# Kernel tuning notes

Hardware: AMD Instinct MI355X
Metric: run time of the kernel (lower is better)

The kernel has to match this reference:

```python
import jax, jax.numpy as jnp
import numpy as np

N_EDGES = 4096
HIDDEN = 256
EDGE_DIM = 128
NUM_HEADS = 4
NUM_GRAPHS = 64


def setup_inputs() -> dict:
    key0 = jax.random.key(0)
    ks = jax.random.split(key0, 10)
    s = 0.02
    inp = {
        "query": jax.random.normal(ks[0], (N_EDGES, HIDDEN), jnp.float32),
        "key": jax.random.normal(ks[1], (N_EDGES, EDGE_DIM), jnp.float32),
        "value": jax.random.normal(ks[2], (N_EDGES, EDGE_DIM), jnp.float32),
        "edge_graph_index": jnp.sort(
            jax.random.randint(ks[3], (N_EDGES,), 0, NUM_GRAPHS)
        ),
        # edge_proj: Linear(edge_context_dim -> hidden_dim)
        "w_edge": jax.random.normal(ks[4], (HIDDEN, EDGE_DIM), jnp.float32) * s,
        "b_edge": jnp.zeros((HIDDEN,), jnp.float32),
        # nn.MultiheadAttention packed in-projection [3H, H] and bias [3H]
        "w_in": jax.random.normal(ks[5], (3 * HIDDEN, HIDDEN), jnp.float32) * s,
        "b_in": jnp.zeros((3 * HIDDEN,), jnp.float32),
        # out_proj: Linear(hidden -> hidden)
        "w_out": jax.random.normal(ks[6], (HIDDEN, HIDDEN), jnp.float32) * s,
        "b_out": jnp.zeros((HIDDEN,), jnp.float32),
    }
    return inp


def reference(query, key, value, edge_graph_index,
              w_edge, b_edge, w_in, b_in, w_out, b_out):
    # Segment-wise cross attention == block-diagonal masked attention over all edges.
    N, H = query.shape
    nh = NUM_HEADS
    dh = H // nh

    # edge feature projection (applied to both key and value, as in the module)
    K = key @ w_edge.T + b_edge      # [N, H]
    V = value @ w_edge.T + b_edge    # [N, H]

    wq, wk, wv = jnp.split(w_in, 3, axis=0)
    bq, bk, bv = jnp.split(b_in, 3)
    Qh = (query @ wq.T + bq).reshape(N, nh, dh)
    Kh = (K @ wk.T + bk).reshape(N, nh, dh)
    Vh = (V @ wv.T + bv).reshape(N, nh, dh)

    scale = 1.0 / jnp.sqrt(jnp.asarray(dh, query.dtype))
    scores = jnp.einsum("nhd,mhd->hnm", Qh, Kh) * scale  # [nh, N, N]

    # attention only within the same graph segment
    same_graph = edge_graph_index[:, None] == edge_graph_index[None, :]  # [N, N]
    neg = jnp.finfo(scores.dtype).min
    scores = jnp.where(same_graph[None, :, :], scores, neg)

    attn = jax.nn.softmax(scores, axis=-1)                 # [nh, N, N]
    out = jnp.einsum("hnm,mhd->nhd", attn, Vh).reshape(N, H)
    out = out @ w_out.T + b_out
    return query + out
```

## Files before the change

### kernel.cpp

```cpp
#include <hip/hip_runtime.h>

#define N_EDGES 4096
#define HIDDEN  256
#define EDGE_DIM 128
#define NUM_HEADS 4
#define NUM_GRAPHS 64
#define DH 64

typedef __attribute__((ext_vector_type(8))) short short8;
typedef __attribute__((ext_vector_type(4))) float f32x4;

__device__ __forceinline__ unsigned short f2bf(float f) {
  unsigned u = __builtin_bit_cast(unsigned, f);
  u += 0x7FFF + ((u >> 16) & 1);
  return (unsigned short)(u >> 16);
}
__device__ __forceinline__ float bf2f(unsigned short u) {
  return __builtin_bit_cast(float, (unsigned)u << 16);
}
__device__ __forceinline__ short8 cvt8(float4 x, float4 y) {
  short8 v;
  v[0] = (short)f2bf(x.x); v[1] = (short)f2bf(x.y);
  v[2] = (short)f2bf(x.z); v[3] = (short)f2bf(x.w);
  v[4] = (short)f2bf(y.x); v[5] = (short)f2bf(y.y);
  v[6] = (short)f2bf(y.z); v[7] = (short)f2bf(y.w);
  return v;
}
__device__ __forceinline__ float4 us4f(ushort4 v) {
  float4 f;
  f.x = bf2f(v.x); f.y = bf2f(v.y); f.z = bf2f(v.z); f.w = bf2f(v.w);
  return f;
}

__device__ __forceinline__ int lbound(const int* __restrict__ a, int n, int v) {
  int lo = 0, hi = n;
  while (lo < hi) { int mid = (lo + hi) >> 1; if (a[mid] < v) lo = mid + 1; else hi = mid; }
  return lo;
}

template<bool ABF, bool OUTF32>
__device__ __forceinline__ void gemm_core(const void* Ap, const float* W,
                                          const float* bias, const float* res,
                                          void* Cp, const int K) {
  const int t = threadIdx.x;
  const int m0 = blockIdx.x * 64, n0 = blockIdx.y * 64;
  __shared__ unsigned short As[64 * 40];
  __shared__ unsigned short Ws[64 * 40];
  const int r = t >> 2, kg = t & 3;
  const int lane = t & 63, w = t >> 6;
  const int quad = lane >> 4, l16 = lane & 15;
  const int wm = (w >> 1) * 32, wn = (w & 1) * 32;
  f32x4 acc[2][2] = {};
  const float* pw = W + (size_t)(n0 + r) * K + kg * 8;
  float4 w0 = *(const float4*)(pw), w1 = *(const float4*)(pw + 4);
  const unsigned short* pa16 = (const unsigned short*)Ap + (size_t)(m0 + r) * K + kg * 8;
  const float* pa32 = (const float*)Ap + (size_t)(m0 + r) * K + kg * 8;
  short8 a16; float4 a0, a1;
  if (ABF) a16 = *(const short8*)pa16;
  else { a0 = *(const float4*)pa32; a1 = *(const float4*)(pa32 + 4); }
  for (int kc = 0; kc < K; kc += 32) {
    short8 na16; float4 na0, na1, nw0, nw1;
    if (kc + 32 < K) {
      if (ABF) na16 = *(const short8*)(pa16 + kc + 32);
      else { na0 = *(const float4*)(pa32 + kc + 32); na1 = *(const float4*)(pa32 + kc + 36); }
      nw0 = *(const float4*)(pw + kc + 32); nw1 = *(const float4*)(pw + kc + 36);
    }
    __syncthreads();
    short8 av = ABF ? a16 : cvt8(a0, a1);
    *(short8*)&As[r * 40 + kg * 8] = av;
    *(short8*)&Ws[r * 40 + kg * 8] = cvt8(w0, w1);
    __syncthreads();
    short8 af0 = *(const short8*)&As[(wm + l16) * 40 + quad * 8];
    short8 af1 = *(const short8*)&As[(wm + 16 + l16) * 40 + quad * 8];
    short8 bf0 = *(const short8*)&Ws[(wn + l16) * 40 + quad * 8];
    short8 bf1 = *(const short8*)&Ws[(wn + 16 + l16) * 40 + quad * 8];
    acc[0][0] = __builtin_amdgcn_mfma_f32_16x16x32_bf16(af0, bf0, acc[0][0], 0, 0, 0);
    acc[0][1] = __builtin_amdgcn_mfma_f32_16x16x32_bf16(af0, bf1, acc[0][1], 0, 0, 0);
    acc[1][0] = __builtin_amdgcn_mfma_f32_16x16x32_bf16(af1, bf0, acc[1][0], 0, 0, 0);
    acc[1][1] = __builtin_amdgcn_mfma_f32_16x16x32_bf16(af1, bf1, acc[1][1], 0, 0, 0);
    a16 = na16; a0 = na0; a1 = na1; w0 = nw0; w1 = nw1;
  }
#pragma unroll
  for (int j = 0; j < 2; ++j) {
    const int col = n0 + wn + j * 16 + l16;
    const float bj = bias[col];
#pragma unroll
    for (int i = 0; i < 2; ++i) {
#pragma unroll
      for (int reg = 0; reg < 4; ++reg) {
        const int row = m0 + wm + i * 16 + quad * 4 + reg;
        const size_t idx = (size_t)row * HIDDEN + col;
        float v = acc[i][j][reg] + bj;
        if (OUTF32) ((float*)Cp)[idx] = v + res[idx];
        else        ((unsigned short*)Cp)[idx] = f2bf(v);
      }
    }
  }
}

__global__ __launch_bounds__(256) void proj1(const float* __restrict__ query,
                                             const float* __restrict__ key,
                                             const float* __restrict__ value,
                                             const float* __restrict__ w_in,
                                             const float* __restrict__ b_in,
                                             const float* __restrict__ w_edge,
                                             const float* __restrict__ b_edge,
                                             const int* __restrict__ gidx,
                                             unsigned short* Qh, unsigned short* Ek,
                                             unsigned short* Ev, int* segStart) {
  if (blockIdx.z == 0 && blockIdx.x == 0 && blockIdx.y == 0 && threadIdx.x <= NUM_GRAPHS)
    segStart[threadIdx.x] = lbound(gidx, N_EDGES, threadIdx.x);
  if (blockIdx.z == 0)      gemm_core<false, false>(query, w_in,   b_in,   nullptr, Qh, 256);
  else if (blockIdx.z == 1) gemm_core<false, false>(key,   w_edge, b_edge, nullptr, Ek, 128);
  else                      gemm_core<false, false>(value, w_edge, b_edge, nullptr, Ev, 128);
}

__global__ __launch_bounds__(256) void proj2(const unsigned short* __restrict__ Ek,
                                             const unsigned short* __restrict__ Ev,
                                             const float* __restrict__ w_in,
                                             const float* __restrict__ b_in,
                                             unsigned short* Kh, unsigned short* Vh) {
  if (blockIdx.z == 0) gemm_core<true, false>(Ek, w_in + 256 * HIDDEN, b_in + 256, nullptr, Kh, 256);
  else                 gemm_core<true, false>(Ev, w_in + 512 * HIDDEN, b_in + 512, nullptr, Vh, 256);
}

__global__ __launch_bounds__(256) void attn_segment(const unsigned short* __restrict__ Qh,
                                                    const unsigned short* __restrict__ Kh,
                                                    const unsigned short* __restrict__ Vh,
                                                    const int* __restrict__ segStart,
                                                    unsigned short* __restrict__ ao) {
  const int graph = blockIdx.x, h = blockIdx.y, zg = blockIdx.z;
  const int segLo = segStart[graph];
  const int segHi = segStart[graph + 1];
  const int segLen = segHi - segLo;
  const int t = threadIdx.x, lane = t & 63, w = t >> 6;
  __shared__ float Qs[16][68], Ks[64][68], Vs[64][68];
  __shared__ float Ps[4][64][4];
  const float scale = 0.125f;
  const int r0 = w * 4;

  for (int chunk = zg; chunk * 16 < segLen; chunk += 8) {
    const int row0 = segLo + chunk * 16;
    const int rows = min(16, segHi - row0);
    __syncthreads();
    { int r = t >> 4, d4 = (t & 15) * 4;
      if (r < rows)
        *(float4*)&Qs[r][d4] =
            us4f(*(const ushort4*)(Qh + (size_t)(row0 + r) * HIDDEN + h * DH + d4)); }

    float accv[4] = {0.f, 0.f, 0.f, 0.f}, lsum[4] = {0.f, 0.f, 0.f, 0.f};

    for (int c0 = segLo; c0 < segHi; c0 += 64) {
      const int tc = min(64, segHi - c0);
      __syncthreads();
#pragma unroll
      for (int it = 0; it < 4; ++it) {
        int s = t + it * 256; int j = s >> 4; int d4 = (s & 15) * 4;
        if (j < tc) {
          *(float4*)&Ks[j][d4] =
              us4f(*(const ushort4*)(Kh + (size_t)(c0 + j) * HIDDEN + h * DH + d4));
          *(float4*)&Vs[j][d4] =
              us4f(*(const ushort4*)(Vh + (size_t)(c0 + j) * HIDDEN + h * DH + d4));
        }
      }
      __syncthreads();
      float4 kreg[16];
#pragma unroll
      for (int d4 = 0; d4 < 16; ++d4) kreg[d4] = *(const float4*)&Ks[lane][d4 * 4];
      float p[4];
#pragma unroll
      for (int r = 0; r < 4; ++r) {
        float s = 0.f;
#pragma unroll
        for (int d4 = 0; d4 < 16; ++d4) {
          float4 q = *(const float4*)&Qs[r0 + r][d4 * 4];
          s += q.x * kreg[d4].x + q.y * kreg[d4].y + q.z * kreg[d4].z + q.w * kreg[d4].w;
        }
        p[r] = (lane < tc && r0 + r < rows) ? __expf(s * scale) : 0.f;
        lsum[r] += p[r];
      }
      float4 p4; p4.x = p[0]; p4.y = p[1]; p4.z = p[2]; p4.w = p[3];
      *(float4*)&Ps[w][lane][0] = p4;
      __asm__ volatile("s_waitcnt lgkmcnt(0)" ::: "memory");
      for (int j = 0; j < tc; ++j) {
        const float v = Vs[j][lane];
        float4 pj = *(const float4*)&Ps[w][j][0];
        accv[0] += pj.x * v; accv[1] += pj.y * v;
        accv[2] += pj.z * v; accv[3] += pj.w * v;
      }
    }
#pragma unroll
    for (int off = 32; off; off >>= 1)
#pragma unroll
      for (int r = 0; r < 4; ++r) lsum[r] += __shfl_xor(lsum[r], off);
#pragma unroll
    for (int r = 0; r < 4; ++r)
      if (r0 + r < rows)
        ao[(size_t)(row0 + r0 + r) * HIDDEN + h * DH + lane] = f2bf(accv[r] / lsum[r]);
  }
}

__global__ __launch_bounds__(256) void outproj(const unsigned short* __restrict__ ao,
                                               const float* __restrict__ w_out,
                                               const float* __restrict__ b_out,
                                               const float* __restrict__ query,
                                               float* __restrict__ out) {
  gemm_core<true, true>(ao, w_out, b_out, query, out, 256);
}

extern "C" void kernel_launch(void* const* d_in, const int* in_sizes, int n_in,
                              void* d_out, int out_size, void* d_ws, size_t ws_size,
                              hipStream_t stream) {
  const float* query  = (const float*)d_in[0];
  const float* key    = (const float*)d_in[1];
  const float* value  = (const float*)d_in[2];
  const int*   gidx   = (const int*)d_in[3];
  const float* w_edge = (const float*)d_in[4];
  const float* b_edge = (const float*)d_in[5];
  const float* w_in   = (const float*)d_in[6];
  const float* b_in   = (const float*)d_in[7];
  const float* w_out  = (const float*)d_in[8];
  const float* b_out  = (const float*)d_in[9];
  float* out = (float*)d_out;

  int* segStart = (int*)d_ws;
  unsigned short* Qh = (unsigned short*)((char*)d_ws + 512);
  unsigned short* Ek = Qh + (size_t)N_EDGES * HIDDEN;
  unsigned short* Ev = Ek + (size_t)N_EDGES * HIDDEN;
  unsigned short* Kh = Ev + (size_t)N_EDGES * HIDDEN;
  unsigned short* Vh = Kh + (size_t)N_EDGES * HIDDEN;
  unsigned short* ao = Vh + (size_t)N_EDGES * HIDDEN;

  proj1<<<dim3(64, 4, 3), 256, 0, stream>>>(query, key, value, w_in, b_in,
                                            w_edge, b_edge, gidx, Qh, Ek, Ev, segStart);
  proj2<<<dim3(64, 4, 2), 256, 0, stream>>>(Ek, Ev, w_in, b_in, Kh, Vh);
  attn_segment<<<dim3(NUM_GRAPHS, NUM_HEADS, 8), 256, 0, stream>>>(Qh, Kh, Vh, segStart, ao);
  outproj<<<dim3(64, 4), 256, 0, stream>>>(ao, w_out, b_out, query, out);
}
```

Measured before the change: 117.7 us.

## Fold edge and in-projections per block, fuse out-projection into attention via atomics

The K/V path now multiplies the two weight matrices inside each block (W_in_k @ W_edge, with a folded bias) and applies the product directly to key/value. This removes the separate proj2 launch and the intermediate Ek/Ev buffers. The output projection is fused into the attention kernel: each head chunk multiplies its bf16 output by the matching slice of w_out and atomically adds into out, which proj pre-initialises with query plus b_out. The change drops two launches and two round trips through global memory, but every block recomputes the weight product, fp32 atomics add contention, and accumulation order becomes nondeterministic.

```diff
diff --git a/kernel.cpp b/kernel.cpp
--- a/kernel.cpp
+++ b/kernel.cpp
@@ -38,10 +38,9 @@
   return lo;
 }
 
-template<bool ABF, bool OUTF32>
-__device__ __forceinline__ void gemm_core(const void* Ap, const float* W,
-                                          const float* bias, const float* res,
-                                          void* Cp, const int K) {
+__device__ __forceinline__ void gemm_core(const float* Ap, const float* W,
+                                          const float* bias, unsigned short* Cp,
+                                          const int K) {
   const int t = threadIdx.x;
   const int m0 = blockIdx.x * 64, n0 = blockIdx.y * 64;
   __shared__ unsigned short As[64 * 40];
@@ -53,21 +52,16 @@
   f32x4 acc[2][2] = {};
   const float* pw = W + (size_t)(n0 + r) * K + kg * 8;
   float4 w0 = *(const float4*)(pw), w1 = *(const float4*)(pw + 4);
-  const unsigned short* pa16 = (const unsigned short*)Ap + (size_t)(m0 + r) * K + kg * 8;
-  const float* pa32 = (const float*)Ap + (size_t)(m0 + r) * K + kg * 8;
-  short8 a16; float4 a0, a1;
-  if (ABF) a16 = *(const short8*)pa16;
-  else { a0 = *(const float4*)pa32; a1 = *(const float4*)(pa32 + 4); }
+  const float* pa32 = Ap + (size_t)(m0 + r) * K + kg * 8;
+  float4 a0 = *(const float4*)pa32, a1 = *(const float4*)(pa32 + 4);
   for (int kc = 0; kc < K; kc += 32) {
-    short8 na16; float4 na0, na1, nw0, nw1;
+    float4 na0, na1, nw0, nw1;
     if (kc + 32 < K) {
-      if (ABF) na16 = *(const short8*)(pa16 + kc + 32);
-      else { na0 = *(const float4*)(pa32 + kc + 32); na1 = *(const float4*)(pa32 + kc + 36); }
-      nw0 = *(const float4*)(pw + kc + 32); nw1 = *(const float4*)(pw + kc + 36);
-    }
-    __syncthreads();
-    short8 av = ABF ? a16 : cvt8(a0, a1);
-    *(short8*)&As[r * 40 + kg * 8] = av;
+      na0 = *(const float4*)(pa32 + kc + 32); na1 = *(const float4*)(pa32 + kc + 36);
+      nw0 = *(const float4*)(pw + kc + 32);   nw1 = *(const float4*)(pw + kc + 36);
+    }
+    __syncthreads();
+    *(short8*)&As[r * 40 + kg * 8] = cvt8(a0, a1);
     *(short8*)&Ws[r * 40 + kg * 8] = cvt8(w0, w1);
     __syncthreads();
     short8 af0 = *(const short8*)&As[(wm + l16) * 40 + quad * 8];
@@ -78,7 +72,7 @@
     acc[0][1] = __builtin_amdgcn_mfma_f32_16x16x32_bf16(af0, bf1, acc[0][1], 0, 0, 0);
     acc[1][0] = __builtin_amdgcn_mfma_f32_16x16x32_bf16(af1, bf0, acc[1][0], 0, 0, 0);
     acc[1][1] = __builtin_amdgcn_mfma_f32_16x16x32_bf16(af1, bf1, acc[1][1], 0, 0, 0);
-    a16 = na16; a0 = na0; a1 = na1; w0 = nw0; w1 = nw1;
+    a0 = na0; a1 = na1; w0 = nw0; w1 = nw1;
   }
 #pragma unroll
   for (int j = 0; j < 2; ++j) {
@@ -89,53 +83,164 @@
 #pragma unroll
       for (int reg = 0; reg < 4; ++reg) {
         const int row = m0 + wm + i * 16 + quad * 4 + reg;
-        const size_t idx = (size_t)row * HIDDEN + col;
-        float v = acc[i][j][reg] + bj;
-        if (OUTF32) ((float*)Cp)[idx] = v + res[idx];
-        else        ((unsigned short*)Cp)[idx] = f2bf(v);
-      }
-    }
-  }
-}
-
-__global__ __launch_bounds__(256) void proj1(const float* __restrict__ query,
-                                             const float* __restrict__ key,
-                                             const float* __restrict__ value,
-                                             const float* __restrict__ w_in,
-                                             const float* __restrict__ b_in,
-                                             const float* __restrict__ w_edge,
-                                             const float* __restrict__ b_edge,
-                                             const int* __restrict__ gidx,
-                                             unsigned short* Qh, unsigned short* Ek,
-                                             unsigned short* Ev, int* segStart) {
-  if (blockIdx.z == 0 && blockIdx.x == 0 && blockIdx.y == 0 && threadIdx.x <= NUM_GRAPHS)
-    segStart[threadIdx.x] = lbound(gidx, N_EDGES, threadIdx.x);
-  if (blockIdx.z == 0)      gemm_core<false, false>(query, w_in,   b_in,   nullptr, Qh, 256);
-  else if (blockIdx.z == 1) gemm_core<false, false>(key,   w_edge, b_edge, nullptr, Ek, 128);
-  else                      gemm_core<false, false>(value, w_edge, b_edge, nullptr, Ev, 128);
-}
-
-__global__ __launch_bounds__(256) void proj2(const unsigned short* __restrict__ Ek,
-                                             const unsigned short* __restrict__ Ev,
-                                             const float* __restrict__ w_in,
-                                             const float* __restrict__ b_in,
-                                             unsigned short* Kh, unsigned short* Vh) {
-  if (blockIdx.z == 0) gemm_core<true, false>(Ek, w_in + 256 * HIDDEN, b_in + 256, nullptr, Kh, 256);
-  else                 gemm_core<true, false>(Ev, w_in + 512 * HIDDEN, b_in + 512, nullptr, Vh, 256);
+        Cp[(size_t)row * HIDDEN + col] = f2bf(acc[i][j][reg] + bj);
+      }
+    }
+  }
+}
+
+__device__ __forceinline__ void fused_kv_core(const float* __restrict__ A,
+                                              const float* __restrict__ Wp,
+                                              const float* __restrict__ bp,
+                                              const float* __restrict__ w_edge,
+                                              const float* __restrict__ b_edge,
+                                              unsigned short* __restrict__ C) {
+  const int t = threadIdx.x;
+  const int m0 = blockIdx.x * 64, n0 = blockIdx.y * 64;
+  __shared__ unsigned short As2[64 * 40];
+  __shared__ unsigned short Bs2[64 * 40];
+  __shared__ unsigned short WfS[64][136];
+  __shared__ float bfS[64];
+  const int r = t >> 2, kg = t & 3;
+  const int lane = t & 63, w = t >> 6;
+  const int quad = lane >> 4, l16 = lane & 15;
+  const int wm = (w >> 1) * 32, wn = (w & 1) * 32;
+
+  {
+    float s = 0.f;
+    const float* wrow = Wp + (size_t)(n0 + r) * HIDDEN + kg * 64;
+    const float* be = b_edge + kg * 64;
+#pragma unroll
+    for (int j = 0; j < 64; j += 4) {
+      float4 a = *(const float4*)(wrow + j);
+      float4 b = *(const float4*)(be + j);
+      s += a.x * b.x + a.y * b.y + a.z * b.z + a.w * b.w;
+    }
+    s += __shfl_xor(s, 1); s += __shfl_xor(s, 2);
+    if (kg == 0) bfS[r] = s + bp[n0 + r];
+  }
+
+#pragma unroll
+  for (int kt = 0; kt < 2; ++kt) {
+    f32x4 facc[2][2] = {};
+    for (int j0 = 0; j0 < HIDDEN; j0 += 32) {
+      __syncthreads();
+      {
+        const float* p = Wp + (size_t)(n0 + r) * HIDDEN + j0 + kg * 8;
+        float4 a0 = *(const float4*)p, a1 = *(const float4*)(p + 4);
+        *(short8*)&As2[r * 40 + kg * 8] = cvt8(a0, a1);
+      }
+      {
+        const int j = t >> 3, k8 = (t & 7) * 8;
+        const float* p = w_edge + (size_t)(j0 + j) * EDGE_DIM + kt * 64 + k8;
+        float4 b0 = *(const float4*)p, b1 = *(const float4*)(p + 4);
+        float bb[8] = {b0.x, b0.y, b0.z, b0.w, b1.x, b1.y, b1.z, b1.w};
+#pragma unroll
+        for (int i = 0; i < 8; ++i) Bs2[(k8 + i) * 40 + j] = f2bf(bb[i]);
+      }
+      __syncthreads();
+      short8 af0 = *(const short8*)&As2[(wm + l16) * 40 + quad * 8];
+      short8 af1 = *(const short8*)&As2[(wm + 16 + l16) * 40 + quad * 8];
+      short8 bf0 = *(const short8*)&Bs2[(wn + l16) * 40 + quad * 8];
+      short8 bf1 = *(const short8*)&Bs2[(wn + 16 + l16) * 40 + quad * 8];
+      facc[0][0] = __builtin_amdgcn_mfma_f32_16x16x32_bf16(af0, bf0, facc[0][0], 0, 0, 0);
+      facc[0][1] = __builtin_amdgcn_mfma_f32_16x16x32_bf16(af0, bf1, facc[0][1], 0, 0, 0);
+      facc[1][0] = __builtin_amdgcn_mfma_f32_16x16x32_bf16(af1, bf0, facc[1][0], 0, 0, 0);
+      facc[1][1] = __builtin_amdgcn_mfma_f32_16x16x32_bf16(af1, bf1, facc[1][1], 0, 0, 0);
+    }
+#pragma unroll
+    for (int jj = 0; jj < 2; ++jj)
+#pragma unroll
+      for (int ii = 0; ii < 2; ++ii)
+#pragma unroll
+        for (int reg = 0; reg < 4; ++reg) {
+          const int n = wm + ii * 16 + quad * 4 + reg;
+          const int k = kt * 64 + wn + jj * 16 + l16;
+          WfS[n][k] = f2bf(facc[ii][jj][reg]);
+        }
+  }
+  __syncthreads();
+
+  f32x4 acc[2][2] = {};
+  for (int kc = 0; kc < EDGE_DIM; kc += 32) {
+    __syncthreads();
+    {
+      const float* p = A + (size_t)(m0 + r) * EDGE_DIM + kc + kg * 8;
+      float4 a0 = *(const float4*)p, a1 = *(const float4*)(p + 4);
+      *(short8*)&As2[r * 40 + kg * 8] = cvt8(a0, a1);
+    }
+    __syncthreads();
+    short8 af0 = *(const short8*)&As2[(wm + l16) * 40 + quad * 8];
+    short8 af1 = *(const short8*)&As2[(wm + 16 + l16) * 40 + quad * 8];
+    short8 bf0 = *(const short8*)&WfS[wn + l16][kc + quad * 8];
+    short8 bf1 = *(const short8*)&WfS[wn + 16 + l16][kc + quad * 8];
+    acc[0][0] = __builtin_amdgcn_mfma_f32_16x16x32_bf16(af0, bf0, acc[0][0], 0, 0, 0);
+    acc[0][1] = __builtin_amdgcn_mfma_f32_16x16x32_bf16(af0, bf1, acc[0][1], 0, 0, 0);
+    acc[1][0] = __builtin_amdgcn_mfma_f32_16x16x32_bf16(af1, bf0, acc[1][0], 0, 0, 0);
+    acc[1][1] = __builtin_amdgcn_mfma_f32_16x16x32_bf16(af1, bf1, acc[1][1], 0, 0, 0);
+  }
+#pragma unroll
+  for (int j = 0; j < 2; ++j) {
+    const int coln = wn + j * 16 + l16;
+    const float bj = bfS[coln];
+#pragma unroll
+    for (int i = 0; i < 2; ++i)
+#pragma unroll
+      for (int reg = 0; reg < 4; ++reg) {
+        const int row = m0 + wm + i * 16 + quad * 4 + reg;
+        C[(size_t)row * HIDDEN + n0 + coln] = f2bf(acc[i][j][reg] + bj);
+      }
+  }
+}
+
+__global__ __launch_bounds__(256) void proj(const float* __restrict__ query,
+                                            const float* __restrict__ key,
+                                            const float* __restrict__ value,
+                                            const float* __restrict__ w_in,
+                                            const float* __restrict__ b_in,
+                                            const float* __restrict__ w_edge,
+                                            const float* __restrict__ b_edge,
+                                            const float* __restrict__ b_out,
+                                            const int* __restrict__ gidx,
+                                            unsigned short* Qh, unsigned short* Kh,
+                                            unsigned short* Vh, int* segStart,
+                                            float* __restrict__ out) {
+  if (blockIdx.z == 0) {
+    if (blockIdx.x == 0 && blockIdx.y == 0 && threadIdx.x <= NUM_GRAPHS)
+      segStart[threadIdx.x] = lbound(gidx, N_EDGES, threadIdx.x);
+    gemm_core(query, w_in, b_in, Qh, 256);
+    const int t = threadIdx.x, m0 = blockIdx.x * 64, n0 = blockIdx.y * 64;
+#pragma unroll
+    for (int i = 0; i < 4; ++i) {
+      const int idx = t + i * 256;
+      const int rr = idx >> 4, cc = (idx & 15) * 4;
+      float4 q = *(const float4*)&query[(size_t)(m0 + rr) * HIDDEN + n0 + cc];
+      float4 b = *(const float4*)&b_out[n0 + cc];
+      q.x += b.x; q.y += b.y; q.z += b.z; q.w += b.w;
+      *(float4*)&out[(size_t)(m0 + rr) * HIDDEN + n0 + cc] = q;
+    }
+  } else if (blockIdx.z == 1) {
+    fused_kv_core(key, w_in + 256 * HIDDEN, b_in + 256, w_edge, b_edge, Kh);
+  } else {
+    fused_kv_core(value, w_in + 512 * HIDDEN, b_in + 512, w_edge, b_edge, Vh);
+  }
 }
 
 __global__ __launch_bounds__(256) void attn_segment(const unsigned short* __restrict__ Qh,
                                                     const unsigned short* __restrict__ Kh,
                                                     const unsigned short* __restrict__ Vh,
                                                     const int* __restrict__ segStart,
-                                                    unsigned short* __restrict__ ao) {
+                                                    const float* __restrict__ w_out,
+                                                    float* __restrict__ out) {
   const int graph = blockIdx.x, h = blockIdx.y, zg = blockIdx.z;
   const int segLo = segStart[graph];
   const int segHi = segStart[graph + 1];
   const int segLen = segHi - segLo;
   const int t = threadIdx.x, lane = t & 63, w = t >> 6;
+  const int quad = lane >> 4, l16 = lane & 15;
   __shared__ float Qs[16][68], Ks[64][68], Vs[64][68];
   __shared__ float Ps[4][64][4];
+  __shared__ unsigned short aohS[16][72];
   const float scale = 0.125f;
   const int r0 = w * 4;
 
@@ -193,19 +298,34 @@
     for (int off = 32; off; off >>= 1)
 #pragma unroll
       for (int r = 0; r < 4; ++r) lsum[r] += __shfl_xor(lsum[r], off);
+
 #pragma unroll
     for (int r = 0; r < 4; ++r)
-      if (r0 + r < rows)
-        ao[(size_t)(row0 + r0 + r) * HIDDEN + h * DH + lane] = f2bf(accv[r] / lsum[r]);
-  }
-}
-
-__global__ __launch_bounds__(256) void outproj(const unsigned short* __restrict__ ao,
-                                               const float* __restrict__ w_out,
-                                               const float* __restrict__ b_out,
-                                               const float* __restrict__ query,
-                                               float* __restrict__ out) {
-  gemm_core<true, true>(ao, w_out, b_out, query, out, 256);
+      aohS[r0 + r][lane] = (r0 + r < rows) ? f2bf(accv[r] / lsum[r]) : (unsigned short)0;
+    __syncthreads();
+
+    f32x4 po[4] = {};
+#pragma unroll
+    for (int kc = 0; kc < DH; kc += 32) {
+      short8 af = *(const short8*)&aohS[l16][kc + quad * 8];
+#pragma unroll
+      for (int nt = 0; nt < 4; ++nt) {
+        const int n = w * 64 + nt * 16 + l16;
+        const float* p = w_out + (size_t)n * HIDDEN + h * DH + kc + quad * 8;
+        float4 b0 = *(const float4*)p, b1 = *(const float4*)(p + 4);
+        po[nt] = __builtin_amdgcn_mfma_f32_16x16x32_bf16(af, cvt8(b0, b1), po[nt], 0, 0, 0);
+      }
+    }
+#pragma unroll
+    for (int nt = 0; nt < 4; ++nt)
+#pragma unroll
+      for (int reg = 0; reg < 4; ++reg) {
+        const int rr = quad * 4 + reg;
+        if (rr < rows)
+          atomicAdd(&out[(size_t)(row0 + rr) * HIDDEN + w * 64 + nt * 16 + l16],
+                    po[nt][reg]);
+      }
+  }
 }
 
 extern "C" void kernel_launch(void* const* d_in, const int* in_sizes, int n_in,
@@ -225,15 +345,12 @@
 
   int* segStart = (int*)d_ws;
   unsigned short* Qh = (unsigned short*)((char*)d_ws + 512);
-  unsigned short* Ek = Qh + (size_t)N_EDGES * HIDDEN;
-  unsigned short* Ev = Ek + (size_t)N_EDGES * HIDDEN;
-  unsigned short* Kh = Ev + (size_t)N_EDGES * HIDDEN;
+  unsigned short* Kh = Qh + (size_t)N_EDGES * HIDDEN;
   unsigned short* Vh = Kh + (size_t)N_EDGES * HIDDEN;
-  unsigned short* ao = Vh + (size_t)N_EDGES * HIDDEN;
-
-  proj1<<<dim3(64, 4, 3), 256, 0, stream>>>(query, key, value, w_in, b_in,
-                                            w_edge, b_edge, gidx, Qh, Ek, Ev, segStart);
-  proj2<<<dim3(64, 4, 2), 256, 0, stream>>>(Ek, Ev, w_in, b_in, Kh, Vh);
-  attn_segment<<<dim3(NUM_GRAPHS, NUM_HEADS, 8), 256, 0, stream>>>(Qh, Kh, Vh, segStart, ao);
-  outproj<<<dim3(64, 4), 256, 0, stream>>>(ao, w_out, b_out, query, out);
-}
+
+  proj<<<dim3(64, 4, 3), 256, 0, stream>>>(query, key, value, w_in, b_in,
+                                           w_edge, b_edge, b_out, gidx,
+                                           Qh, Kh, Vh, segStart, out);
+  attn_segment<<<dim3(NUM_GRAPHS, NUM_HEADS, 8), 256, 0, stream>>>(Qh, Kh, Vh, segStart,
+                                                                   w_out, out);
+}
```

Measured after the change: 135.2 us. +14.9%, slower.

## Fold edge projection into K/V in-projection weights and fuse stages into cooperative kernel

Applied to the files above, without the earlier changes.

Precomputes the fused weights Wk·W_edge and Wv·W_edge (plus fused biases) on device, so K and V are produced by a single K=128 GEMM from the raw key/value instead of two chained GEMMs. All stages run inside one persistent cooperative kernel of 512 blocks separated by grid syncs, removing three kernel launch boundaries. The attention work is spread over the persistent blocks in a strided loop. A multi-kernel fallback runs if the cooperative launch fails. It adds the risk of extra bf16 rounding in the fused weights and a dependence on 512 blocks being co-resident.

```diff
diff --git a/kernel.cpp b/kernel.cpp
--- a/kernel.cpp
+++ b/kernel.cpp
@@ -1,4 +1,7 @@
 #include <hip/hip_runtime.h>
+#include <hip/hip_cooperative_groups.h>
+
+namespace cg = cooperative_groups;
 
 #define N_EDGES 4096
 #define HIDDEN  256
@@ -6,6 +9,8 @@
 #define NUM_HEADS 4
 #define NUM_GRAPHS 64
 #define DH 64
+#define NBLK 512
+#define ATTN_UNITS 2048
 
 typedef __attribute__((ext_vector_type(8))) short short8;
 typedef __attribute__((ext_vector_type(4))) float f32x4;
@@ -38,47 +43,54 @@
   return lo;
 }
 
-template<bool ABF, bool OUTF32>
-__device__ __forceinline__ void gemm_core(const void* Ap, const float* W,
-                                          const float* bias, const float* res,
-                                          void* Cp, const int K) {
+union SharedU {
+  struct { unsigned short As[64 * 40]; unsigned short Ws[64 * 40]; } g;
+  struct { float Qs[16][68]; float Ks[64][68]; float Vs[64][68]; float Ps[4][64][4]; } a;
+};
+
+template<bool ABF, bool WBF, bool OUTF32>
+__device__ __forceinline__ void gemm_tile(const void* Ap, const void* Wp,
+                                          const float* __restrict__ bias,
+                                          const float* __restrict__ res,
+                                          void* Cp, const int K,
+                                          const int m0, const int n0,
+                                          unsigned short* As, unsigned short* Ws) {
   const int t = threadIdx.x;
-  const int m0 = blockIdx.x * 64, n0 = blockIdx.y * 64;
-  __shared__ unsigned short As[64 * 40];
-  __shared__ unsigned short Ws[64 * 40];
   const int r = t >> 2, kg = t & 3;
   const int lane = t & 63, w = t >> 6;
   const int quad = lane >> 4, l16 = lane & 15;
   const int wm = (w >> 1) * 32, wn = (w & 1) * 32;
   f32x4 acc[2][2] = {};
-  const float* pw = W + (size_t)(n0 + r) * K + kg * 8;
-  float4 w0 = *(const float4*)(pw), w1 = *(const float4*)(pw + 4);
+  const float*          pa32 = (const float*)Ap          + (size_t)(m0 + r) * K + kg * 8;
   const unsigned short* pa16 = (const unsigned short*)Ap + (size_t)(m0 + r) * K + kg * 8;
-  const float* pa32 = (const float*)Ap + (size_t)(m0 + r) * K + kg * 8;
-  short8 a16; float4 a0, a1;
+  const float*          pw32 = (const float*)Wp          + (size_t)(n0 + r) * K + kg * 8;
+  const unsigned short* pw16 = (const unsigned short*)Wp + (size_t)(n0 + r) * K + kg * 8;
+  short8 a16, w16; float4 a0, a1, w0, w1;
   if (ABF) a16 = *(const short8*)pa16;
   else { a0 = *(const float4*)pa32; a1 = *(const float4*)(pa32 + 4); }
+  if (WBF) w16 = *(const short8*)pw16;
+  else { w0 = *(const float4*)pw32; w1 = *(const float4*)(pw32 + 4); }
   for (int kc = 0; kc < K; kc += 32) {
-    short8 na16; float4 na0, na1, nw0, nw1;
+    short8 na16, nw16; float4 na0, na1, nw0, nw1;
     if (kc + 32 < K) {
       if (ABF) na16 = *(const short8*)(pa16 + kc + 32);
       else { na0 = *(const float4*)(pa32 + kc + 32); na1 = *(const float4*)(pa32 + kc + 36); }
-      nw0 = *(const float4*)(pw + kc + 32); nw1 = *(const float4*)(pw + kc + 36);
+      if (WBF) nw16 = *(const short8*)(pw16 + kc + 32);
+      else { nw0 = *(const float4*)(pw32 + kc + 32); nw1 = *(const float4*)(pw32 + kc + 36); }
     }
     __syncthreads();
-    short8 av = ABF ? a16 : cvt8(a0, a1);
-    *(short8*)&As[r * 40 + kg * 8] = av;
-    *(short8*)&Ws[r * 40 + kg * 8] = cvt8(w0, w1);
+    *(short8*)&As[r * 40 + kg * 8] = ABF ? a16 : cvt8(a0, a1);
+    *(short8*)&Ws[r * 40 + kg * 8] = WBF ? w16 : cvt8(w0, w1);
     __syncthreads();
     short8 af0 = *(const short8*)&As[(wm + l16) * 40 + quad * 8];
     short8 af1 = *(const short8*)&As[(wm + 16 + l16) * 40 + quad * 8];
-    short8 bf0 = *(const short8*)&Ws[(wn + l16) * 40 + quad * 8];
-    short8 bf1 = *(const short8*)&Ws[(wn + 16 + l16) * 40 + quad * 8];
-    acc[0][0] = __builtin_amdgcn_mfma_f32_16x16x32_bf16(af0, bf0, acc[0][0], 0, 0, 0);
-    acc[0][1] = __builtin_amdgcn_mfma_f32_16x16x32_bf16(af0, bf1, acc[0][1], 0, 0, 0);
-    acc[1][0] = __builtin_amdgcn_mfma_f32_16x16x32_bf16(af1, bf0, acc[1][0], 0, 0, 0);
-    acc[1][1] = __builtin_amdgcn_mfma_f32_16x16x32_bf16(af1, bf1, acc[1][1], 0, 0, 0);
-    a16 = na16; a0 = na0; a1 = na1; w0 = nw0; w1 = nw1;
+    short8 bq0 = *(const short8*)&Ws[(wn + l16) * 40 + quad * 8];
+    short8 bq1 = *(const short8*)&Ws[(wn + 16 + l16) * 40 + quad * 8];
+    acc[0][0] = __builtin_amdgcn_mfma_f32_16x16x32_bf16(af0, bq0, acc[0][0], 0, 0, 0);
+    acc[0][1] = __builtin_amdgcn_mfma_f32_16x16x32_bf16(af0, bq1, acc[0][1], 0, 0, 0);
+    acc[1][0] = __builtin_amdgcn_mfma_f32_16x16x32_bf16(af1, bq0, acc[1][0], 0, 0, 0);
+    acc[1][1] = __builtin_amdgcn_mfma_f32_16x16x32_bf16(af1, bq1, acc[1][1], 0, 0, 0);
+    a16 = na16; a0 = na0; a1 = na1; w16 = nw16; w0 = nw0; w1 = nw1;
   }
 #pragma unroll
   for (int j = 0; j < 2; ++j) {
@@ -98,44 +110,85 @@
   }
 }
 
-__global__ __launch_bounds__(256) void proj1(const float* __restrict__ query,
-                                             const float* __restrict__ key,
-                                             const float* __restrict__ value,
-                                             const float* __restrict__ w_in,
-                                             const float* __restrict__ b_in,
-                                             const float* __restrict__ w_edge,
-                                             const float* __restrict__ b_edge,
-                                             const int* __restrict__ gidx,
-                                             unsigned short* Qh, unsigned short* Ek,
-                                             unsigned short* Ev, int* segStart) {
-  if (blockIdx.z == 0 && blockIdx.x == 0 && blockIdx.y == 0 && threadIdx.x <= NUM_GRAPHS)
-    segStart[threadIdx.x] = lbound(gidx, N_EDGES, threadIdx.x);
-  if (blockIdx.z == 0)      gemm_core<false, false>(query, w_in,   b_in,   nullptr, Qh, 256);
-  else if (blockIdx.z == 1) gemm_core<false, false>(key,   w_edge, b_edge, nullptr, Ek, 128);
-  else                      gemm_core<false, false>(value, w_edge, b_edge, nullptr, Ev, 128);
-}
-
-__global__ __launch_bounds__(256) void proj2(const unsigned short* __restrict__ Ek,
-                                             const unsigned short* __restrict__ Ev,
-                                             const float* __restrict__ w_in,
-                                             const float* __restrict__ b_in,
-                                             unsigned short* Kh, unsigned short* Vh) {
-  if (blockIdx.z == 0) gemm_core<true, false>(Ek, w_in + 256 * HIDDEN, b_in + 256, nullptr, Kh, 256);
-  else                 gemm_core<true, false>(Ev, w_in + 512 * HIDDEN, b_in + 512, nullptr, Vh, 256);
-}
-
-__global__ __launch_bounds__(256) void attn_segment(const unsigned short* __restrict__ Qh,
-                                                    const unsigned short* __restrict__ Kh,
-                                                    const unsigned short* __restrict__ Vh,
-                                                    const int* __restrict__ segStart,
-                                                    unsigned short* __restrict__ ao) {
-  const int graph = blockIdx.x, h = blockIdx.y, zg = blockIdx.z;
+__device__ __forceinline__ void wf_part(int bb, const float* __restrict__ w_in,
+                                        const float* __restrict__ b_in,
+                                        const float* __restrict__ w_edge,
+                                        const float* __restrict__ b_edge,
+                                        unsigned short* __restrict__ Wfk,
+                                        unsigned short* __restrict__ Wfv,
+                                        float* __restrict__ bfk, float* __restrict__ bfv,
+                                        unsigned short* As, unsigned short* Bs) {
+  const int sel = bb >> 3;
+  const int tt  = bb & 7;
+  const int n0  = (tt >> 1) * 64;
+  const int k0  = (tt & 1) * 64;
+  const float* Wp = w_in + (size_t)(256 + 256 * sel) * HIDDEN;
+  const float* bp = b_in + 256 + 256 * sel;
+  unsigned short* Wf = sel ? Wfv : Wfk;
+  float* bf = sel ? bfv : bfk;
+  const int t = threadIdx.x;
+  const int r = t >> 2, kg = t & 3;
+  const int lane = t & 63, w = t >> 6;
+  const int quad = lane >> 4, l16 = lane & 15;
+  const int wm = (w >> 1) * 32, wn = (w & 1) * 32;
+  if (k0 == 0) {
+    float s = 0.f;
+    const float* wrow = Wp + (size_t)(n0 + r) * HIDDEN + kg * 64;
+    const float* be = b_edge + kg * 64;
+#pragma unroll
+    for (int j = 0; j < 64; j += 4) {
+      float4 a = *(const float4*)(wrow + j);
+      float4 b = *(const float4*)(be + j);
+      s += a.x * b.x + a.y * b.y + a.z * b.z + a.w * b.w;
+    }
+    s += __shfl_xor(s, 1); s += __shfl_xor(s, 2);
+    if (kg == 0) bf[n0 + r] = s + bp[n0 + r];
+  }
+  f32x4 facc[2][2] = {};
+  for (int j0 = 0; j0 < HIDDEN; j0 += 32) {
+    __syncthreads();
+    { const float* p = Wp + (size_t)(n0 + r) * HIDDEN + j0 + kg * 8;
+      float4 x0 = *(const float4*)p, x1 = *(const float4*)(p + 4);
+      *(short8*)&As[r * 40 + kg * 8] = cvt8(x0, x1); }
+    { const int j = t >> 3, k8 = (t & 7) * 8;
+      const float* p = w_edge + (size_t)(j0 + j) * EDGE_DIM + k0 + k8;
+      float4 b0 = *(const float4*)p, b1 = *(const float4*)(p + 4);
+      float bv[8] = {b0.x, b0.y, b0.z, b0.w, b1.x, b1.y, b1.z, b1.w};
+#pragma unroll
+      for (int i = 0; i < 8; ++i) Bs[(k8 + i) * 40 + j] = f2bf(bv[i]); }
+    __syncthreads();
+    short8 af0 = *(const short8*)&As[(wm + l16) * 40 + quad * 8];
+    short8 af1 = *(const short8*)&As[(wm + 16 + l16) * 40 + quad * 8];
+    short8 bq0 = *(const short8*)&Bs[(wn + l16) * 40 + quad * 8];
+    short8 bq1 = *(const short8*)&Bs[(wn + 16 + l16) * 40 + quad * 8];
+    facc[0][0] = __builtin_amdgcn_mfma_f32_16x16x32_bf16(af0, bq0, facc[0][0], 0, 0, 0);
+    facc[0][1] = __builtin_amdgcn_mfma_f32_16x16x32_bf16(af0, bq1, facc[0][1], 0, 0, 0);
+    facc[1][0] = __builtin_amdgcn_mfma_f32_16x16x32_bf16(af1, bq0, facc[1][0], 0, 0, 0);
+    facc[1][1] = __builtin_amdgcn_mfma_f32_16x16x32_bf16(af1, bq1, facc[1][1], 0, 0, 0);
+  }
+#pragma unroll
+  for (int jj = 0; jj < 2; ++jj)
+#pragma unroll
+    for (int ii = 0; ii < 2; ++ii)
+#pragma unroll
+      for (int reg = 0; reg < 4; ++reg) {
+        const int n = wm + ii * 16 + quad * 4 + reg;
+        const int k = wn + jj * 16 + l16;
+        Wf[(size_t)(n0 + n) * EDGE_DIM + k0 + k] = f2bf(facc[ii][jj][reg]);
+      }
+}
+
+__device__ __forceinline__ void attn_unit(int graph, int h, int zg,
+                                          const unsigned short* __restrict__ Qh,
+                                          const unsigned short* __restrict__ Kh,
+                                          const unsigned short* __restrict__ Vh,
+                                          const int* __restrict__ segStart,
+                                          unsigned short* __restrict__ ao,
+                                          SharedU& sh) {
   const int segLo = segStart[graph];
   const int segHi = segStart[graph + 1];
   const int segLen = segHi - segLo;
   const int t = threadIdx.x, lane = t & 63, w = t >> 6;
-  __shared__ float Qs[16][68], Ks[64][68], Vs[64][68];
-  __shared__ float Ps[4][64][4];
   const float scale = 0.125f;
   const int r0 = w * 4;
 
@@ -145,7 +198,7 @@
     __syncthreads();
     { int r = t >> 4, d4 = (t & 15) * 4;
       if (r < rows)
-        *(float4*)&Qs[r][d4] =
+        *(float4*)&sh.a.Qs[r][d4] =
             us4f(*(const ushort4*)(Qh + (size_t)(row0 + r) * HIDDEN + h * DH + d4)); }
 
     float accv[4] = {0.f, 0.f, 0.f, 0.f}, lsum[4] = {0.f, 0.f, 0.f, 0.f};
@@ -157,34 +210,34 @@
       for (int it = 0; it < 4; ++it) {
         int s = t + it * 256; int j = s >> 4; int d4 = (s & 15) * 4;
         if (j < tc) {
-          *(float4*)&Ks[j][d4] =
+          *(float4*)&sh.a.Ks[j][d4] =
               us4f(*(const ushort4*)(Kh + (size_t)(c0 + j) * HIDDEN + h * DH + d4));
-          *(float4*)&Vs[j][d4] =
+          *(float4*)&sh.a.Vs[j][d4] =
               us4f(*(const ushort4*)(Vh + (size_t)(c0 + j) * HIDDEN + h * DH + d4));
         }
       }
       __syncthreads();
       float4 kreg[16];
 #pragma unroll
-      for (int d4 = 0; d4 < 16; ++d4) kreg[d4] = *(const float4*)&Ks[lane][d4 * 4];
+      for (int d4 = 0; d4 < 16; ++d4) kreg[d4] = *(const float4*)&sh.a.Ks[lane][d4 * 4];
       float p[4];
 #pragma unroll
       for (int r = 0; r < 4; ++r) {
         float s = 0.f;
 #pragma unroll
         for (int d4 = 0; d4 < 16; ++d4) {
-          float4 q = *(const float4*)&Qs[r0 + r][d4 * 4];
+          float4 q = *(const float4*)&sh.a.Qs[r0 + r][d4 * 4];
           s += q.x * kreg[d4].x + q.y * kreg[d4].y + q.z * kreg[d4].z + q.w * kreg[d4].w;
         }
         p[r] = (lane < tc && r0 + r < rows) ? __expf(s * scale) : 0.f;
         lsum[r] += p[r];
       }
       float4 p4; p4.x = p[0]; p4.y = p[1]; p4.z = p[2]; p4.w = p[3];
-      *(float4*)&Ps[w][lane][0] = p4;
+      *(float4*)&sh.a.Ps[w][lane][0] = p4;
       __asm__ volatile("s_waitcnt lgkmcnt(0)" ::: "memory");
       for (int j = 0; j < tc; ++j) {
-        const float v = Vs[j][lane];
-        float4 pj = *(const float4*)&Ps[w][j][0];
+        const float v = sh.a.Vs[j][lane];
+        float4 pj = *(const float4*)&sh.a.Ps[w][j][0];
         accv[0] += pj.x * v; accv[1] += pj.y * v;
         accv[2] += pj.z * v; accv[3] += pj.w * v;
       }
@@ -200,12 +253,97 @@
   }
 }
 
-__global__ __launch_bounds__(256) void outproj(const unsigned short* __restrict__ ao,
-                                               const float* __restrict__ w_out,
-                                               const float* __restrict__ b_out,
-                                               const float* __restrict__ query,
-                                               float* __restrict__ out) {
-  gemm_core<true, true>(ao, w_out, b_out, query, out, 256);
+__global__ __launch_bounds__(256, 2) void k_all(
+    const float* __restrict__ query, const float* __restrict__ key,
+    const float* __restrict__ value, const float* __restrict__ w_in,
+    const float* __restrict__ b_in, const float* __restrict__ w_edge,
+    const float* __restrict__ b_edge, const float* __restrict__ w_out,
+    const float* __restrict__ b_out, const int* __restrict__ gidx,
+    int* segStart, unsigned short* Qh, unsigned short* Kh, unsigned short* Vh,
+    unsigned short* ao, unsigned short* Wfk, unsigned short* Wfv,
+    float* bfk, float* bfv, float* out) {
+  __shared__ SharedU sh;
+  const int b = blockIdx.x;
+  cg::grid_group grid = cg::this_grid();
+
+  if (b < 256) {
+    gemm_tile<false, false, false>(query, w_in, b_in, nullptr, Qh, 256,
+                                   (b & 63) * 64, (b >> 6) * 64, sh.g.As, sh.g.Ws);
+  } else if (b < 272) {
+    wf_part(b - 256, w_in, b_in, w_edge, b_edge, Wfk, Wfv, bfk, bfv, sh.g.As, sh.g.Ws);
+  } else if (b == 272) {
+    if (threadIdx.x <= NUM_GRAPHS)
+      segStart[threadIdx.x] = lbound(gidx, N_EDGES, threadIdx.x);
+  }
+  __threadfence();
+  grid.sync();
+
+  {
+    const int sel = b >> 8, rem = b & 255;
+    gemm_tile<false, true, false>(sel ? value : key, sel ? Wfv : Wfk,
+                                  sel ? bfv : bfk, nullptr, sel ? Vh : Kh, 128,
+                                  (rem & 63) * 64, (rem >> 6) * 64, sh.g.As, sh.g.Ws);
+  }
+  __threadfence();
+  grid.sync();
+
+  for (int u = b; u < ATTN_UNITS; u += NBLK)
+    attn_unit(u >> 5, (u >> 3) & 3, u & 7, Qh, Kh, Vh, segStart, ao, sh);
+  __threadfence();
+  grid.sync();
+
+  if (b < 256)
+    gemm_tile<true, false, true>(ao, w_out, b_out, query, out, 256,
+                                 (b & 63) * 64, (b >> 6) * 64, sh.g.As, sh.g.Ws);
+}
+
+__global__ __launch_bounds__(256) void k_p1(
+    const float* __restrict__ query, const float* __restrict__ w_in,
+    const float* __restrict__ b_in, const float* __restrict__ w_edge,
+    const float* __restrict__ b_edge, const int* __restrict__ gidx,
+    int* segStart, unsigned short* Qh, unsigned short* Wfk, unsigned short* Wfv,
+    float* bfk, float* bfv) {
+  __shared__ SharedU sh;
+  const int b = blockIdx.x;
+  if (b < 256)
+    gemm_tile<false, false, false>(query, w_in, b_in, nullptr, Qh, 256,
+                                   (b & 63) * 64, (b >> 6) * 64, sh.g.As, sh.g.Ws);
+  else if (b < 272)
+    wf_part(b - 256, w_in, b_in, w_edge, b_edge, Wfk, Wfv, bfk, bfv, sh.g.As, sh.g.Ws);
+  else if (threadIdx.x <= NUM_GRAPHS)
+    segStart[threadIdx.x] = lbound(gidx, N_EDGES, threadIdx.x);
+}
+
+__global__ __launch_bounds__(256) void k_p2(
+    const float* __restrict__ key, const float* __restrict__ value,
+    const unsigned short* __restrict__ Wfk, const unsigned short* __restrict__ Wfv,
+    const float* __restrict__ bfk, const float* __restrict__ bfv,
+    unsigned short* Kh, unsigned short* Vh) {
+  __shared__ SharedU sh;
+  const int b = blockIdx.x;
+  const int sel = b >> 8, rem = b & 255;
+  gemm_tile<false, true, false>(sel ? value : key, sel ? Wfv : Wfk,
+                                sel ? bfv : bfk, nullptr, sel ? Vh : Kh, 128,
+                                (rem & 63) * 64, (rem >> 6) * 64, sh.g.As, sh.g.Ws);
+}
+
+__global__ __launch_bounds__(256) void k_p3(
+    const unsigned short* __restrict__ Qh, const unsigned short* __restrict__ Kh,
+    const unsigned short* __restrict__ Vh, const int* __restrict__ segStart,
+    unsigned short* __restrict__ ao) {
+  __shared__ SharedU sh;
+  for (int u = blockIdx.x; u < ATTN_UNITS; u += gridDim.x)
+    attn_unit(u >> 5, (u >> 3) & 3, u & 7, Qh, Kh, Vh, segStart, ao, sh);
+}
+
+__global__ __launch_bounds__(256) void k_p4(
+    const unsigned short* __restrict__ ao, const float* __restrict__ w_out,
+    const float* __restrict__ b_out, const float* __restrict__ query,
+    float* __restrict__ out) {
+  __shared__ SharedU sh;
+  const int b = blockIdx.x;
+  gemm_tile<true, false, true>(ao, w_out, b_out, query, out, 256,
+                               (b & 63) * 64, (b >> 6) * 64, sh.g.As, sh.g.Ws);
 }
 
 extern "C" void kernel_launch(void* const* d_in, const int* in_sizes, int n_in,
@@ -224,16 +362,28 @@
   float* out = (float*)d_out;
 
   int* segStart = (int*)d_ws;
-  unsigned short* Qh = (unsigned short*)((char*)d_ws + 512);
-  unsigned short* Ek = Qh + (size_t)N_EDGES * HIDDEN;
-  unsigned short* Ev = Ek + (size_t)N_EDGES * HIDDEN;
-  unsigned short* Kh = Ev + (size_t)N_EDGES * HIDDEN;
-  unsigned short* Vh = Kh + (size_t)N_EDGES * HIDDEN;
-  unsigned short* ao = Vh + (size_t)N_EDGES * HIDDEN;
-
-  proj1<<<dim3(64, 4, 3), 256, 0, stream>>>(query, key, value, w_in, b_in,
-                                            w_edge, b_edge, gidx, Qh, Ek, Ev, segStart);
-  proj2<<<dim3(64, 4, 2), 256, 0, stream>>>(Ek, Ev, w_in, b_in, Kh, Vh);
-  attn_segment<<<dim3(NUM_GRAPHS, NUM_HEADS, 8), 256, 0, stream>>>(Qh, Kh, Vh, segStart, ao);
-  outproj<<<dim3(64, 4), 256, 0, stream>>>(ao, w_out, b_out, query, out);
-}
+  unsigned short* Qh  = (unsigned short*)((char*)d_ws + 512);
+  unsigned short* Kh  = Qh + (size_t)N_EDGES * HIDDEN;
+  unsigned short* Vh  = Kh + (size_t)N_EDGES * HIDDEN;
+  unsigned short* ao  = Vh + (size_t)N_EDGES * HIDDEN;
+  unsigned short* Wfk = ao + (size_t)N_EDGES * HIDDEN;
+  unsigned short* Wfv = Wfk + 256 * EDGE_DIM;
+  float* bfk = (float*)(Wfv + 256 * EDGE_DIM);
+  float* bfv = bfk + 256;
+
+  void* args[] = {(void*)&query, (void*)&key, (void*)&value, (void*)&w_in,
+                  (void*)&b_in, (void*)&w_edge, (void*)&b_edge, (void*)&w_out,
+                  (void*)&b_out, (void*)&gidx, (void*)&segStart, (void*)&Qh,
+                  (void*)&Kh, (void*)&Vh, (void*)&ao, (void*)&Wfk, (void*)&Wfv,
+                  (void*)&bfk, (void*)&bfv, (void*)&out};
+  hipError_t err = hipLaunchCooperativeKernel((void*)k_all, dim3(NBLK), dim3(256),
+                                              (void**)args, 0, stream);
+  if (err != hipSuccess) {
+    (void)hipGetLastError();
+    k_p1<<<dim3(273), 256, 0, stream>>>(query, w_in, b_in, w_edge, b_edge, gidx,
+                                        segStart, Qh, Wfk, Wfv, bfk, bfv);
+    k_p2<<<dim3(512), 256, 0, stream>>>(key, value, Wfk, Wfv, bfk, bfv, Kh, Vh);
+    k_p3<<<dim3(2048), 256, 0, stream>>>(Qh, Kh, Vh, segStart, ao);
+    k_p4<<<dim3(256), 256, 0, stream>>>(ao, w_out, b_out, query, out);
+  }
+}
```

Result: slower. 458.6 us (+289.6%).
